# Kernel tuning notes

Hardware: AMD Instinct MI355X
Metric: run time of the kernel (lower is better)

The kernel has to match this reference:

```python
import jax, jax.numpy as jnp
import numpy as np

B, T, D, H = 64, 512, 512, 128

def swish(x):
    return x * jax.nn.sigmoid(x)

def setup_inputs() -> dict:
    key = jax.random.key(0)
    ks = jax.random.split(key, 8)
    X = jax.random.normal(ks[0], (B, T, D), dtype=jnp.float32)
    # strictly-upper-triangular random binary adjacency -> valid DAG
    adj = jax.random.bernoulli(ks[1], 0.3, (T, T)).astype(jnp.float32)
    dag = jnp.triu(adj, k=1)
    s = 1.0 / np.sqrt(D)
    Wk = jax.random.normal(ks[2], (H, D), dtype=jnp.float32) * s
    bk = jax.random.normal(ks[3], (H,), dtype=jnp.float32) * 0.01
    Wq = jax.random.normal(ks[4], (H, D), dtype=jnp.float32) * s
    bq = jax.random.normal(ks[5], (H,), dtype=jnp.float32) * 0.01
    Wv = jax.random.normal(ks[6], (H, D), dtype=jnp.float32) * s
    bv = jax.random.normal(ks[7], (H,), dtype=jnp.float32) * 0.01
    return {"X": X, "dag": dag, "Wk": Wk, "bk": bk, "Wq": Wq, "bq": bq, "Wv": Wv, "bv": bv}

def reference(X, dag, Wk, bk, Wq, bq, Wv, bv):
    K = swish(jnp.einsum('btd,hd->bth', X, Wk) + bk)  # [B,T,H]
    Q = swish(jnp.einsum('btd,hd->bth', X, Wq) + bq)
    V = swish(jnp.einsum('btd,hd->bth', X, Wv) + bv)
    S_qk = jnp.einsum('bqh,bkh->bqk', Q, K) / jnp.sqrt(jnp.float32(H))  # [B,T,T]
    dagT = dag.T  # [T,T]
    Sprime = dagT * jnp.einsum('ij,bjk->bik', dagT, S_qk)  # [B,T,T]
    # masked_fill(Sprime == 0, -inf) then softmax; rows that are all -inf
    # would produce NaN in torch and are replaced by zeros -> do it nan-free.
    nz = Sprime != 0
    masked = jnp.where(nz, Sprime, -jnp.inf)
    row_valid = jnp.any(nz, axis=-1, keepdims=True)  # [B,T,1]
    masked_safe = jnp.where(row_valid, masked, 0.0)
    probs = jax.nn.softmax(masked_safe, axis=-1) * row_valid  # [B,T,T]
    Vprime = jnp.einsum('ij,bjh->bih', dagT, V)  # [B,T,H]
    O = jnp.einsum('bqk,bkh->bqh', probs, V) + Vprime
    return O
```

## Files before the change

kernel.cpp:

```cpp
#include <hip/hip_runtime.h>
#include <hip/hip_bf16.h>

#define Bn 64
#define Tn 512
#define Dn 512
#define Hn 128
#define BT (Bn*Tn)

typedef unsigned short u16;
typedef unsigned long long u64;
typedef __attribute__((ext_vector_type(8))) short bf16x8;
typedef __attribute__((ext_vector_type(4))) float f32x4;

__device__ __forceinline__ u16 f2bf(float f) {
  union { __hip_bfloat16 h; u16 u; } v;
  v.h = __float2bfloat16(f);
  return v.u;
}

__device__ __forceinline__ bf16x8 pack8(float4 a, float4 b) {
  bf16x8 o;
  o[0] = (short)f2bf(a.x); o[1] = (short)f2bf(a.y);
  o[2] = (short)f2bf(a.z); o[3] = (short)f2bf(a.w);
  o[4] = (short)f2bf(b.x); o[5] = (short)f2bf(b.y);
  o[6] = (short)f2bf(b.z); o[7] = (short)f2bf(b.w);
  return o;
}

__device__ __forceinline__ void gload16(const void* g, void* lds) {
  __builtin_amdgcn_global_load_lds(
      (const __attribute__((address_space(1))) unsigned int*)g,
      (__attribute__((address_space(3))) unsigned int*)lds, 16, 0, 0);
}

__global__ __launch_bounds__(256) void prep(
    const float4* __restrict__ Wk, const float4* __restrict__ Wq,
    const float4* __restrict__ Wv, ushort4* __restrict__ Wcat,
    const float* __restrict__ dag, u16* __restrict__ dagT,
    u64* __restrict__ bits) {
  __shared__ float s[64][65];
  if (blockIdx.x < 192) {
    int idx = blockIdx.x * 256 + threadIdx.x;
    int which = idx >> 14, j = idx & 16383;
    const float4* src = (which == 0) ? Wk : (which == 1) ? Wq : Wv;
    float4 v = src[j];
    ushort4 o; o.x = f2bf(v.x); o.y = f2bf(v.y); o.z = f2bf(v.z); o.w = f2bf(v.w);
    Wcat[idx] = o;
  } else {
    int bid = blockIdx.x - 192;
    int bx = bid & 7, by = bid >> 3;
    int r0 = by * 64, c0 = bx * 64;
    int t = threadIdx.x;
    int c4 = t & 15, rr = t >> 4;
#pragma unroll
    for (int q = 0; q < 4; ++q) {
      int r = rr + q * 16;
      float4 v = *(const float4*)&dag[(size_t)(r0 + r) * Tn + c0 + c4 * 4];
      s[c4 * 4 + 0][r] = v.x; s[c4 * 4 + 1][r] = v.y;
      s[c4 * 4 + 2][r] = v.z; s[c4 * 4 + 3][r] = v.w;
    }
    __syncthreads();
#pragma unroll
    for (int q = 0; q < 4; ++q) {
      int il = rr + q * 16;
      ushort4 o;
      u64 b4 = 0;
#pragma unroll
      for (int r = 0; r < 4; ++r) {
        float v = s[il][c4 * 4 + r];
        ((u16*)&o)[r] = f2bf(v);
        b4 |= (u64)(v != 0.f) << (c4 * 4 + r);
      }
      *(ushort4*)&dagT[(size_t)(c0 + il) * Tn + r0 + c4 * 4] = o;
      b4 |= __shfl_xor(b4, 1, 64);
      b4 |= __shfl_xor(b4, 2, 64);
      b4 |= __shfl_xor(b4, 4, 64);
      b4 |= __shfl_xor(b4, 8, 64);
      if (c4 == 0) bits[(size_t)(c0 + il) * 8 + (r0 >> 6)] = b4;
    }
  }
}

__global__ __launch_bounds__(256, 2) void qkv3(
    const float* __restrict__ X, const u16* __restrict__ Wcat,
    const float* __restrict__ bk, const float* __restrict__ bq,
    const float* __restrict__ bv,
    u16* __restrict__ Kb, u16* __restrict__ QT, u16* __restrict__ VT) {
  __shared__ u16 sm[28672];
  int bid = blockIdx.x;
  int xcd = bid & 7, idx = bid >> 3;
  int b = (idx & 7) * 8 + xcd;
  int rowblk = idx >> 3;
  int m0 = b * Tn + rowblk * 64;
  int tid = threadIdx.x, lane = tid & 63, wave = tid >> 6;
  int col0 = lane & 15, rg = lane >> 4, kcb = rg * 16;
  int swl = (col0 & 7) << 4;
  int xrow = tid >> 2, xcq = tid & 3;
  f32x4 acc[3][4][2] = {};
  const char* Wb = (const char*)Wcat;
  char* smb = (char*)sm;

#define LOAD_X(kt_)                                                             \
  {                                                                             \
    const float4* s_ = (const float4*)(X + (size_t)(m0 + xrow) * Dn + (kt_) + xcq * 16); \
    xa0 = s_[0]; xa1 = s_[1]; xa2 = s_[2]; xa3 = s_[3];                         \
  }

  float4 xa0, xa1, xa2, xa3;
  LOAD_X(0);
  for (int kt = 0; kt < Dn; kt += 64) {
    {
      int sw = (xrow & 7) << 4;
      *(bf16x8*)(smb + xrow * 128 + ((xcq * 32) ^ sw)) = pack8(xa0, xa1);
      *(bf16x8*)(smb + xrow * 128 + ((xcq * 32 + 16) ^ sw)) = pack8(xa2, xa3);
    }
    if (kt + 64 < Dn) LOAD_X(kt + 64);
#pragma unroll
    for (int q = 0; q < 12; ++q) {
      int c2 = wave * 12 + q;
      int which = c2 >> 4, widx = c2 & 15;
      int flat = widx * 1024 + lane * 16;
      int row = flat >> 7, colb = flat & 127;
      int sw = (row & 7) << 4;
      gload16(Wb + (size_t)which * 131072 + (size_t)row * 1024 + (kt << 1) + (colb ^ sw),
              smb + 8192 + which * 16384 + widx * 1024);
    }
    __syncthreads();
    bf16x8 af[4][2];
#pragma unroll
    for (int m = 0; m < 4; ++m)
#pragma unroll
      for (int kk = 0; kk < 2; ++kk)
        af[m][kk] = *(const bf16x8*)(smb + (m * 16 + col0) * 128 + ((kk * 64 + kcb) ^ swl));
#pragma unroll
    for (int which = 0; which < 3; ++which) {
      bf16x8 bfr[2][2];
#pragma unroll
      for (int n = 0; n < 2; ++n)
#pragma unroll
        for (int kk = 0; kk < 2; ++kk)
          bfr[n][kk] = *(const bf16x8*)(smb + 8192 + which * 16384 +
                                        (wave * 32 + n * 16 + col0) * 128 + ((kk * 64 + kcb) ^ swl));
#pragma unroll
      for (int kk = 0; kk < 2; ++kk)
#pragma unroll
        for (int m = 0; m < 4; ++m)
#pragma unroll
          for (int n = 0; n < 2; ++n)
            acc[which][m][n] = __builtin_amdgcn_mfma_f32_16x16x32_bf16(
                af[m][kk], bfr[n][kk], acc[which][m][n], 0, 0, 0);
    }
    __syncthreads();
  }
#undef LOAD_X

  {
#pragma unroll
    for (int n = 0; n < 2; ++n) {
      int nl = wave * 32 + n * 16 + col0;
      float bsk = bk[nl], bsq = bq[nl], bsv = bv[nl];
#pragma unroll
      for (int m = 0; m < 4; ++m)
#pragma unroll
        for (int r = 0; r < 4; ++r) {
          int tl = m * 16 + rg * 4 + r;
          float xk = acc[0][m][n][r] + bsk;
          float xq = acc[1][m][n][r] + bsq;
          float xv = acc[2][m][n][r] + bsv;
          *(u16*)(smb + tl * 256 + ((nl * 2) ^ ((tl & 7) << 4))) = f2bf(xk / (1.f + __expf(-xk)));
          *(u16*)(smb + 16384 + nl * 128 + ((tl * 2) ^ ((nl & 7) << 4))) = f2bf(xq / (1.f + __expf(-xq)));
          *(u16*)(smb + 32768 + nl * 128 + ((tl * 2) ^ ((nl & 7) << 4))) = f2bf(xv / (1.f + __expf(-xv)));
        }
    }
    __syncthreads();
    int tt0 = rowblk * 64;
#pragma unroll
    for (int p = 0; p < 4; ++p) {
      int c = p * 256 + tid;
      int t = c >> 4, c16 = c & 15;
      *(bf16x8*)&Kb[(size_t)(m0 + t) * Hn + c16 * 8] =
          *(const bf16x8*)(smb + t * 256 + ((c16 * 16) ^ ((t & 7) << 4)));
    }
#pragma unroll
    for (int p = 0; p < 4; ++p) {
      int c = p * 256 + tid;
      int h = c >> 3, c8 = c & 7;
      *(bf16x8*)&QT[((size_t)b * Hn + h) * Tn + tt0 + c8 * 8] =
          *(const bf16x8*)(smb + 16384 + h * 128 + ((c8 * 16) ^ ((h & 7) << 4)));
      *(bf16x8*)&VT[((size_t)b * Hn + h) * Tn + tt0 + c8 * 8] =
          *(const bf16x8*)(smb + 32768 + h * 128 + ((c8 * 16) ^ ((h & 7) << 4)));
    }
  }
}

__global__ __launch_bounds__(512, 4) void dattn(
    const u16* __restrict__ dagT, const u16* __restrict__ QT,
    const u16* __restrict__ VT, const u16* __restrict__ Kb,
    const u64* __restrict__ dbits, float* __restrict__ O) {
  __shared__ char smA[65536];
  __shared__ u16 smQ2[8192];

  int bid = blockIdx.x;
  int xcd = bid & 7, rst = bid >> 3;
  int bx = rst & 7, b = (rst >> 3) * 8 + xcd;
  int m0 = bx * 64;
  int tid = threadIdx.x, lane = tid & 63, wave = tid >> 6;
  int col0 = lane & 15, g = lane >> 4;
  int swl = (col0 & 7) << 4;
  int grp = wave >> 2, gw = wave & 3;

  const char* Ab = (const char*)(dagT + (size_t)m0 * Tn);
  const char* Qb = (const char*)(QT + (size_t)b * Hn * Tn);
  const char* Vb = (const char*)(VT + (size_t)b * Hn * Tn);
  const char* Kb0 = (const char*)(Kb + (size_t)b * Tn * Hn);

  f32x4 accq[4] = {};
  for (int kt = 0; kt < Tn; kt += 64) {
    {
      int ch = wave;
      int flat = ch * 1024 + lane * 16;
      int row = flat >> 7, colb = flat & 127;
      int sw = (row & 7) << 4;
      gload16(Ab + (size_t)row * 1024 + kt * 2 + (colb ^ sw), smA + ch * 1024);
    }
#pragma unroll
    for (int q = 0; q < 2; ++q) {
      int ch = wave * 2 + q;
      int flat = ch * 1024 + lane * 16;
      int row = flat >> 7, colb = flat & 127;
      int sw = (row & 7) << 4;
      gload16(Qb + (size_t)row * 1024 + kt * 2 + (colb ^ sw), smA + 8192 + ch * 1024);
    }
    __syncthreads();
    bf16x8 af[4][2], fq[2];
#pragma unroll
    for (int m = 0; m < 4; ++m)
#pragma unroll
      for (int kk = 0; kk < 2; ++kk)
        af[m][kk] = *(const bf16x8*)(smA + (m * 16 + col0) * 128 + ((kk * 64 + g * 16) ^ swl));
#pragma unroll
    for (int kk = 0; kk < 2; ++kk)
      fq[kk] = *(const bf16x8*)(smA + 8192 + (wave * 16 + col0) * 128 + ((kk * 64 + g * 16) ^ swl));
#pragma unroll
    for (int kk = 0; kk < 2; ++kk)
#pragma unroll
      for (int m = 0; m < 4; ++m)
        accq[m] = __builtin_amdgcn_mfma_f32_16x16x32_bf16(af[m][kk], fq[kk], accq[m], 0, 0, 0);
    __syncthreads();
  }

  const float scale = 0.08838834764831845f;
#pragma unroll
  for (int m = 0; m < 4; ++m)
#pragma unroll
    for (int r = 0; r < 4; ++r) {
      int q = m * 16 + g * 4 + r;
      int h = wave * 16 + col0;
      *(u16*)((char*)smQ2 + q * 256 + ((h * 2) ^ ((q & 7) << 4))) = f2bf(accq[m][r] * scale);
    }

#define STAGE_K(c_)                                                            \
  {                                                                            \
    _Pragma("unroll")                                                          \
    for (int q = 0; q < 4; ++q) {                                              \
      int ch = gw * 4 + q;                                                     \
      int flat = ch * 1024 + lane * 16;                                        \
      int row = flat >> 8, colb = flat & 255;                                  \
      gload16(Kb0 + (size_t)(grp * 256 + (c_) * 64 + row) * 256 + (colb ^ ((row & 7) << 4)), \
              smA + grp * 32768 + ((c_) & 1) * 16384 + ch * 1024);             \
    }                                                                          \
  }

  STAGE_K(0);
  __syncthreads();

  int qrow = gw * 16 + col0;
  bf16x8 bq[4];
#pragma unroll
  for (int kk = 0; kk < 4; ++kk)
    bq[kk] = *(const bf16x8*)((char*)smQ2 + qrow * 256 + ((kk * 64 + g * 16) ^ ((qrow & 7) << 4)));
  const u64* dbq = dbits + (size_t)(m0 + qrow) * 8;
  u64 md[4];
#pragma unroll
  for (int w = 0; w < 4; ++w) md[w] = dbq[grp * 4 + w];

  f32x4 sa[16] = {};
#pragma unroll
  for (int c = 0; c < 4; ++c) {
    if (c < 3) STAGE_K(c + 1);
    const char* kb = smA + grp * 32768 + (c & 1) * 16384;
#pragma unroll
    for (int t = 0; t < 4; ++t)
#pragma unroll
      for (int kk = 0; kk < 4; ++kk) {
        bf16x8 ak = *(const bf16x8*)(kb + (t * 16 + col0) * 256 + ((kk * 64 + g * 16) ^ swl));
        sa[c * 4 + t] = __builtin_amdgcn_mfma_f32_16x16x32_bf16(ak, bq[kk], sa[c * 4 + t], 0, 0, 0);
      }
    if (c < 3) __syncthreads();
  }

  float mx = -INFINITY;
#pragma unroll
  for (int c = 0; c < 4; ++c)
#pragma unroll
    for (int t = 0; t < 4; ++t)
#pragma unroll
      for (int r = 0; r < 4; ++r) {
        int bit = t * 16 + g * 4 + r;
        float v = ((md[c] >> bit) & 1) ? sa[c * 4 + t][r] : -INFINITY;
        sa[c * 4 + t][r] = v;
        mx = fmaxf(mx, v);
      }
  mx = fmaxf(mx, __shfl_xor(mx, 16, 64));
  mx = fmaxf(mx, __shfl_xor(mx, 32, 64));

  float* redf = (float*)smQ2;
  __syncthreads();
  if (g == 0) redf[qrow * 2 + grp] = mx;
  __syncthreads();
  float mboth = fmaxf(redf[qrow * 2], redf[qrow * 2 + 1]);
  float mm = (mboth == -INFINITY) ? 0.f : mboth;

  float s = 0.f;
#pragma unroll
  for (int i = 0; i < 16; ++i)
#pragma unroll
    for (int r = 0; r < 4; ++r) {
      float v = sa[i][r];
      float e = (v == -INFINITY) ? 0.f : __expf(v - mm);
      sa[i][r] = e;
      s += e;
    }
  s += __shfl_xor(s, 16, 64);
  s += __shfl_xor(s, 32, 64);
  if (g == 0) redf[128 + qrow * 2 + grp] = s;
  __syncthreads();
  float stot = redf[128 + qrow * 2] + redf[128 + qrow * 2 + 1];
  float inv = (stot > 0.f) ? (1.f / stot) : 0.f;

  ushort4 pk[16];
#pragma unroll
  for (int c = 0; c < 4; ++c)
#pragma unroll
    for (int t = 0; t < 4; ++t) {
      ushort4 p;
#pragma unroll
      for (int r = 0; r < 4; ++r) {
        int bit = t * 16 + g * 4 + r;
        float d = (float)((md[c] >> bit) & 1);
        ((u16*)&p)[r] = f2bf(sa[c * 4 + t][r] * inv + d);
      }
      pk[c * 4 + t] = p;
    }

  f32x4 acco[4] = {};
  int sww = (qrow & 7) << 4;

#define WRITE_P(c_, base_)                                                     \
  if (grp == ((c_) >> 1)) {                                                    \
    int cc = (c_) & 1;                                                         \
    _Pragma("unroll")                                                          \
    for (int u = 0; u < 2; ++u)                                                \
      _Pragma("unroll")                                                        \
      for (int t2 = 0; t2 < 4; ++t2)                                           \
        *(ushort4*)((base_) + qrow * 256 + ((u * 128 + t2 * 32 + g * 8) ^ sww)) = \
            pk[(cc * 2 + u) * 4 + t2];                                         \
  }

  __syncthreads();
  WRITE_P(0, smA);
  __syncthreads();
#pragma unroll
  for (int c = 0; c < 4; ++c) {
    const char* pb = smA + (c & 1) * 16384;
    if (c < 3) WRITE_P(c + 1, smA + ((c + 1) & 1) * 16384);
#pragma unroll
    for (int kk = 0; kk < 4; ++kk) {
      bf16x8 pa[4], vb;
#pragma unroll
      for (int m = 0; m < 4; ++m) {
        int row = m * 16 + col0;
        pa[m] = *(const bf16x8*)(pb + row * 256 + ((kk * 64 + g * 16) ^ ((row & 7) << 4)));
      }
      vb = *(const bf16x8*)(Vb + (size_t)(wave * 16 + col0) * 1024 + c * 256 + kk * 64 + g * 16);
#pragma unroll
      for (int m = 0; m < 4; ++m)
        acco[m] = __builtin_amdgcn_mfma_f32_16x16x32_bf16(pa[m], vb, acco[m], 0, 0, 0);
    }
    __syncthreads();
  }

#pragma unroll
  for (int m = 0; m < 4; ++m)
#pragma unroll
    for (int r = 0; r < 4; ++r) {
      int i = m0 + m * 16 + g * 4 + r;
      int h = wave * 16 + col0;
      O[((size_t)b * Tn + i) * Hn + h] = acco[m][r];
    }
#undef STAGE_K
#undef WRITE_P
}

extern "C" void kernel_launch(void* const* d_in, const int* in_sizes, int n_in,
                              void* d_out, int out_size, void* d_ws, size_t ws_size,
                              hipStream_t stream) {
  const float* X   = (const float*)d_in[0];
  const float* dag = (const float*)d_in[1];
  const float* Wk  = (const float*)d_in[2];
  const float* bk  = (const float*)d_in[3];
  const float* Wq  = (const float*)d_in[4];
  const float* bq  = (const float*)d_in[5];
  const float* Wv  = (const float*)d_in[6];
  const float* bv  = (const float*)d_in[7];
  float* O = (float*)d_out;

  char* ws = (char*)d_ws;
  u16* Wcat = (u16*)(ws);
  u16* dagT = (u16*)(ws + 393216);
  u64* dbits= (u64*)(ws + 917504);
  u16* Kb   = (u16*)(ws + 950272);
  u16* QT   = (u16*)(ws + 9338880);
  u16* VT   = (u16*)(ws + 17727488);

  prep<<<256, 256, 0, stream>>>((const float4*)Wk, (const float4*)Wq,
                                (const float4*)Wv, (ushort4*)Wcat, dag, dagT, dbits);
  qkv3<<<BT / 64, 256, 0, stream>>>(X, Wcat, bk, bq, bv, Kb, QT, VT);
  dattn<<<512, 512, 0, stream>>>(dagT, QT, VT, Kb, dbits, O);
}
```

Baseline: 65.63 us.

## Shrink qkv3 shared memory by staging one weight matrix at a time

The QKV projection kernel now stages only one of the three weight tiles (K, Q or V) in shared memory per step instead of all three. The epilogue writes K, Q and V through one reused buffer in sequence. This cuts LDS from 56KB to 24KB and raises launch bounds from 2 to 4 blocks per CU for more occupancy. In exchange it adds three times as many barriers per k-step and reloads the A fragments for each weight, and the accumulator registers (96 floats) may limit occupancy anyway.

Result: slower. 109.9 us (+67.5%).

```diff
diff --git a/kernel.cpp b/kernel.cpp
--- a/kernel.cpp
+++ b/kernel.cpp
@@ -81,12 +81,12 @@
   }
 }
 
-__global__ __launch_bounds__(256, 2) void qkv3(
+__global__ __launch_bounds__(256, 4) void qkv3(
     const float* __restrict__ X, const u16* __restrict__ Wcat,
     const float* __restrict__ bk, const float* __restrict__ bq,
     const float* __restrict__ bv,
     u16* __restrict__ Kb, u16* __restrict__ QT, u16* __restrict__ VT) {
-  __shared__ u16 sm[28672];
+  __shared__ u16 sm[12288];
   int bid = blockIdx.x;
   int xcd = bid & 7, idx = bid >> 3;
   int b = (idx & 7) * 8 + xcd;
@@ -105,41 +105,47 @@
     const float4* s_ = (const float4*)(X + (size_t)(m0 + xrow) * Dn + (kt_) + xcq * 16); \
     xa0 = s_[0]; xa1 = s_[1]; xa2 = s_[2]; xa3 = s_[3];                         \
   }
+#define PACK_X()                                                                \
+  {                                                                             \
+    int sw_ = (xrow & 7) << 4;                                                  \
+    *(bf16x8*)(smb + xrow * 128 + ((xcq * 32) ^ sw_)) = pack8(xa0, xa1);        \
+    *(bf16x8*)(smb + xrow * 128 + ((xcq * 32 + 16) ^ sw_)) = pack8(xa2, xa3);   \
+  }
+#define STAGE_W(which_, kt_)                                                    \
+  {                                                                             \
+    _Pragma("unroll")                                                           \
+    for (int q = 0; q < 4; ++q) {                                               \
+      int ch = wave * 4 + q;                           \
+      int flat = ch * 1024 + lane * 16;                                         \
+      int row = flat >> 7, colb = flat & 127;                                   \
+      int sw_ = (row & 7) << 4;                                                 \
+      gload16(Wb + (size_t)(which_) * 131072 + (size_t)row * 1024 + ((kt_) << 1) + (colb ^ sw_), \
+              smb + 8192 + ch * 1024);                                          \
+    }                                                                           \
+  }
 
   float4 xa0, xa1, xa2, xa3;
   LOAD_X(0);
+  PACK_X();
+  LOAD_X(64);
+
   for (int kt = 0; kt < Dn; kt += 64) {
-    {
-      int sw = (xrow & 7) << 4;
-      *(bf16x8*)(smb + xrow * 128 + ((xcq * 32) ^ sw)) = pack8(xa0, xa1);
-      *(bf16x8*)(smb + xrow * 128 + ((xcq * 32 + 16) ^ sw)) = pack8(xa2, xa3);
-    }
-    if (kt + 64 < Dn) LOAD_X(kt + 64);
-#pragma unroll
-    for (int q = 0; q < 12; ++q) {
-      int c2 = wave * 12 + q;
-      int which = c2 >> 4, widx = c2 & 15;
-      int flat = widx * 1024 + lane * 16;
-      int row = flat >> 7, colb = flat & 127;
-      int sw = (row & 7) << 4;
-      gload16(Wb + (size_t)which * 131072 + (size_t)row * 1024 + (kt << 1) + (colb ^ sw),
-              smb + 8192 + which * 16384 + widx * 1024);
-    }
-    __syncthreads();
-    bf16x8 af[4][2];
-#pragma unroll
-    for (int m = 0; m < 4; ++m)
-#pragma unroll
-      for (int kk = 0; kk < 2; ++kk)
-        af[m][kk] = *(const bf16x8*)(smb + (m * 16 + col0) * 128 + ((kk * 64 + kcb) ^ swl));
 #pragma unroll
     for (int which = 0; which < 3; ++which) {
+      STAGE_W(which, kt);
+      __syncthreads();
+      bf16x8 af[4][2];
+#pragma unroll
+      for (int m = 0; m < 4; ++m)
+#pragma unroll
+        for (int kk = 0; kk < 2; ++kk)
+          af[m][kk] = *(const bf16x8*)(smb + (m * 16 + col0) * 128 + ((kk * 64 + kcb) ^ swl));
       bf16x8 bfr[2][2];
 #pragma unroll
       for (int n = 0; n < 2; ++n)
 #pragma unroll
         for (int kk = 0; kk < 2; ++kk)
-          bfr[n][kk] = *(const bf16x8*)(smb + 8192 + which * 16384 +
+          bfr[n][kk] = *(const bf16x8*)(smb + 8192 +
                                         (wave * 32 + n * 16 + col0) * 128 + ((kk * 64 + kcb) ^ swl));
 #pragma unroll
       for (int kk = 0; kk < 2; ++kk)
@@ -149,31 +155,33 @@
           for (int n = 0; n < 2; ++n)
             acc[which][m][n] = __builtin_amdgcn_mfma_f32_16x16x32_bf16(
                 af[m][kk], bfr[n][kk], acc[which][m][n], 0, 0, 0);
-    }
-    __syncthreads();
+      __syncthreads();
+      if (which == 2 && kt + 64 < Dn) {
+        PACK_X();
+        if (kt + 128 < Dn) LOAD_X(kt + 128);
+      }
+    }
   }
 #undef LOAD_X
-
+#undef PACK_X
+#undef STAGE_W
+
+  int tt0 = rowblk * 64;
   {
 #pragma unroll
     for (int n = 0; n < 2; ++n) {
       int nl = wave * 32 + n * 16 + col0;
-      float bsk = bk[nl], bsq = bq[nl], bsv = bv[nl];
+      float bs = bk[nl];
 #pragma unroll
       for (int m = 0; m < 4; ++m)
 #pragma unroll
         for (int r = 0; r < 4; ++r) {
           int tl = m * 16 + rg * 4 + r;
-          float xk = acc[0][m][n][r] + bsk;
-          float xq = acc[1][m][n][r] + bsq;
-          float xv = acc[2][m][n][r] + bsv;
-          *(u16*)(smb + tl * 256 + ((nl * 2) ^ ((tl & 7) << 4))) = f2bf(xk / (1.f + __expf(-xk)));
-          *(u16*)(smb + 16384 + nl * 128 + ((tl * 2) ^ ((nl & 7) << 4))) = f2bf(xq / (1.f + __expf(-xq)));
-          *(u16*)(smb + 32768 + nl * 128 + ((tl * 2) ^ ((nl & 7) << 4))) = f2bf(xv / (1.f + __expf(-xv)));
+          float x = acc[0][m][n][r] + bs;
+          *(u16*)(smb + tl * 256 + ((nl * 2) ^ ((tl & 7) << 4))) = f2bf(x / (1.f + __expf(-x)));
         }
     }
     __syncthreads();
-    int tt0 = rowblk * 64;
 #pragma unroll
     for (int p = 0; p < 4; ++p) {
       int c = p * 256 + tid;
@@ -181,14 +189,32 @@
       *(bf16x8*)&Kb[(size_t)(m0 + t) * Hn + c16 * 8] =
           *(const bf16x8*)(smb + t * 256 + ((c16 * 16) ^ ((t & 7) << 4)));
     }
+  }
+#pragma unroll
+  for (int which = 1; which < 3; ++which) {
+    const float* bias = (which == 1) ? bq : bv;
+    u16* dst = (which == 1) ? QT : VT;
+    __syncthreads();
+#pragma unroll
+    for (int n = 0; n < 2; ++n) {
+      int nl = wave * 32 + n * 16 + col0;
+      float bs = bias[nl];
+#pragma unroll
+      for (int m = 0; m < 4; ++m)
+#pragma unroll
+        for (int r = 0; r < 4; ++r) {
+          int tl = m * 16 + rg * 4 + r;
+          float x = acc[which][m][n][r] + bs;
+          *(u16*)(smb + nl * 128 + ((tl * 2) ^ ((nl & 7) << 4))) = f2bf(x / (1.f + __expf(-x)));
+        }
+    }
+    __syncthreads();
 #pragma unroll
     for (int p = 0; p < 4; ++p) {
       int c = p * 256 + tid;
       int h = c >> 3, c8 = c & 7;
-      *(bf16x8*)&QT[((size_t)b * Hn + h) * Tn + tt0 + c8 * 8] =
-          *(const bf16x8*)(smb + 16384 + h * 128 + ((c8 * 16) ^ ((h & 7) << 4)));
-      *(bf16x8*)&VT[((size_t)b * Hn + h) * Tn + tt0 + c8 * 8] =
-          *(const bf16x8*)(smb + 32768 + h * 128 + ((c8 * 16) ^ ((h & 7) << 4)));
+      *(bf16x8*)&dst[((size_t)b * Hn + h) * Tn + tt0 + c8 * 8] =
+          *(const bf16x8*)(smb + h * 128 + ((c8 * 16) ^ ((h & 7) << 4)));
     }
   }
 }
```
